# Kernel tuning notes

Hardware: AMD Instinct MI355X
Metric: run time of the kernel (lower is better)

The kernel has to match this reference:

```python
import jax, jax.numpy as jnp
import numpy as np

N = 100000      # nodes
E = 2000000     # edges
F_NODE = 32     # num_node_features
F_EDGE = 16     # num_edge_features
HID = 128       # size_conv_layers
G = 4096        # num graphs (molecules)
NCLS = 2        # class_weights.shape[0]
NEG = 0.01      # LeakyReLU default negative slope
BN_EPS = 1e-5


def _bn(h, gamma, beta):
    # torch BatchNorm1d training-mode forward: biased batch stats over node dim
    m = jnp.mean(h, axis=0)
    v = jnp.var(h, axis=0)
    return (h - m) * jax.lax.rsqrt(v + BN_EPS) * gamma + beta


def _lrelu(h):
    return jnp.where(h > 0, h, NEG * h)


def setup_inputs() -> dict:
    key = jax.random.key(0)
    ks = jax.random.split(key, 64)
    d = {}
    d["x"] = jax.random.normal(ks[0], (N, F_NODE), dtype=jnp.float32)
    d["edge_index"] = jax.random.randint(ks[1], (2, E), 0, N, dtype=jnp.int64)
    d["edge_attr"] = jax.random.normal(ks[2], (E, F_EDGE), dtype=jnp.float32)
    d["batch"] = jnp.sort(jax.random.randint(ks[3], (N,), 0, G, dtype=jnp.int64))
    dims = [F_NODE, HID, HID]  # in_channels of each conv layer
    i = 4
    for l, ic in enumerate(dims):
        d[f"eps{l}"] = jnp.zeros((), jnp.float32)                                # GINE train_eps init 0
        d[f"ew{l}"] = 0.05 * jax.random.normal(ks[i], (F_EDGE, ic), jnp.float32); i += 1
        d[f"eb{l}"] = jnp.zeros((ic,), jnp.float32)
        d[f"w1{l}"] = 0.05 * jax.random.normal(ks[i], (ic, HID), jnp.float32); i += 1
        d[f"b1{l}"] = jnp.zeros((HID,), jnp.float32)
        d[f"g1{l}"] = jnp.ones((HID,), jnp.float32)
        d[f"be1{l}"] = jnp.zeros((HID,), jnp.float32)
        d[f"w2{l}"] = 0.05 * jax.random.normal(ks[i], (HID, HID), jnp.float32); i += 1
        d[f"b2{l}"] = jnp.zeros((HID,), jnp.float32)
        d[f"g2{l}"] = jnp.ones((HID,), jnp.float32)
        d[f"be2{l}"] = jnp.zeros((HID,), jnp.float32)
    d["wf"] = 0.05 * jax.random.normal(ks[i], (2 * HID, NCLS), jnp.float32)
    d["bf"] = jnp.zeros((NCLS,), jnp.float32)
    return d


def _forward(x, edge_index, edge_attr, batch, layers, wf, bf):
    src = edge_index[0]  # x_j (messages flow source->target in PyG)
    dst = edge_index[1]  # x_i
    for (eps, ew, eb, w1, b1, g1, be1, w2, b2, g2, be2) in layers:
        e = edge_attr @ ew + eb                     # [E, in_ch]
        msg = jax.nn.relu(x[src] + e)               # GINE message
        agg = jax.ops.segment_sum(msg, dst, num_segments=N)
        h = (1.0 + eps) * x + agg                   # [N, in_ch]
        h = _lrelu(_bn(h @ w1 + b1, g1, be1))       # nn: Lin->BN->LeakyReLU
        h = h @ w2 + b2                             # nn: Lin
        x = _lrelu(_bn(h, g2, be2))                 # outer BN + LeakyReLU
    pool = jax.ops.segment_sum(x, batch, num_segments=G)  # global_add_pool
    x_cat = jnp.concatenate([x, pool[batch]], axis=1)      # repeat_interleave broadcast
    logits = x_cat @ wf + bf
    return jax.nn.softmax(logits, axis=1)


def reference(x, edge_index, edge_attr, batch,
              eps0, ew0, eb0, w10, b10, g10, be10, w20, b20, g20, be20,
              eps1, ew1, eb1, w11, b11, g11, be11, w21, b21, g21, be21,
              eps2, ew2, eb2, w12, b12, g12, be12, w22, b22, g22, be22,
              wf, bf):
    layers = [
        (eps0, ew0, eb0, w10, b10, g10, be10, w20, b20, g20, be20),
        (eps1, ew1, eb1, w11, b11, g11, be11, w21, b21, g21, be21),
        (eps2, ew2, eb2, w12, b12, g12, be12, w22, b22, g22, be22),
    ]
    return _forward(x, edge_index, edge_attr, batch, layers, wf, bf)
```

## Files before the change

### kernel.cpp

```cpp
#include <hip/hip_runtime.h>

#define GEMM_GRID 512
#define GNUM 4096

typedef __attribute__((ext_vector_type(8))) short short8_t;
typedef __attribute__((ext_vector_type(4))) float f32x4;
typedef __attribute__((ext_vector_type(2))) float v2f;

__device__ __forceinline__ float bf2f(unsigned short u) {
    union { unsigned int i; float f; } v; v.i = ((unsigned int)u) << 16; return v.f;
}
__device__ __forceinline__ unsigned short f2bf(float f) {
    union { float f; unsigned int i; } v; v.f = f;
    unsigned int b = v.i + 0x7FFFu + ((v.i >> 16) & 1u);
    return (unsigned short)(b >> 16);
}
__device__ __forceinline__ float lrelu(float v) { return v > 0.f ? v : 0.01f * v; }

__global__ __launch_bounds__(256) void hist_kernel(
    const int* __restrict__ dstv, int* __restrict__ cnt, int E)
{
    int i = blockIdx.x * 256 + threadIdx.x;
    if (i < E) atomicAdd(&cnt[dstv[i] + 1], 1);
}

__global__ __launch_bounds__(256) void scan_block_kernel(
    int* __restrict__ data, int* __restrict__ bsum, int n)
{
    __shared__ int s[256];
    int tid = threadIdx.x;
    int base = blockIdx.x * 1024 + tid * 4;
    int v[4]; int run = 0;
    #pragma unroll
    for (int i = 0; i < 4; i++) {
        int x = (base + i < n) ? data[base + i] : 0;
        run += x; v[i] = run;
    }
    s[tid] = run; __syncthreads();
    for (int off = 1; off < 256; off <<= 1) {
        int t = (tid >= off) ? s[tid - off] : 0;
        __syncthreads();
        s[tid] += t;
        __syncthreads();
    }
    int excl = s[tid] - run;
    #pragma unroll
    for (int i = 0; i < 4; i++)
        if (base + i < n) data[base + i] = v[i] + excl;
    if (tid == 255) bsum[blockIdx.x] = s[255];
}

__global__ __launch_bounds__(128) void scan_carry_kernel(int* __restrict__ bsum, int nb)
{
    __shared__ int s[128];
    int tid = threadIdx.x;
    int orig = (tid < nb) ? bsum[tid] : 0;
    s[tid] = orig; __syncthreads();
    for (int off = 1; off < 128; off <<= 1) {
        int t = (tid >= off) ? s[tid - off] : 0;
        __syncthreads();
        s[tid] += t;
        __syncthreads();
    }
    if (tid < nb) bsum[tid] = s[tid] - orig;
}

__global__ __launch_bounds__(256) void scan_add_kernel(
    int* __restrict__ data, const int* __restrict__ bsum,
    int* __restrict__ cursor, int n, int N)
{
    int i = blockIdx.x * 256 + threadIdx.x;
    if (i < n) {
        int v = data[i] + bsum[i >> 10];
        data[i] = v;
        if (i < N) cursor[i] = v;
    }
}

__global__ __launch_bounds__(256) void scatter_kernel(
    const int* __restrict__ dstv, int* __restrict__ cursor,
    int* __restrict__ perm, int E)
{
    int i = blockIdx.x * 256 + threadIdx.x;
    if (i < E) {
        int p = atomicAdd(&cursor[dstv[i]], 1);
        perm[p] = i;
    }
}

__global__ __launch_bounds__(256) void reorder_kernel(
    const float* __restrict__ ea, const int* __restrict__ srcv,
    const int* __restrict__ perm, float* __restrict__ eap,
    int* __restrict__ srcp, int E)
{
    int i = blockIdx.x * 256 + threadIdx.x;
    int p = i >> 2, q = i & 3;
    if (p >= E) return;
    int e = perm[p];
    float4 v = reinterpret_cast<const float4*>(ea)[e * 4 + q];
    reinterpret_cast<float4*>(eap)[p * 4 + q] = v;
    if (q == 0) srcp[p] = srcv[e];
}

template<bool RO>
__global__ __launch_bounds__(256) void gather_kernel32(
    const float* __restrict__ ea, const int* __restrict__ srcv,
    const int* __restrict__ perm, const int* __restrict__ off,
    const float* __restrict__ ew, const float* __restrict__ ebias,
    const float* __restrict__ epsp, const float* __restrict__ x,
    unsigned short* __restrict__ aggh, unsigned short* __restrict__ aggl, int N)
{
    __shared__ float ebuf[4][32 * 16];
    const int tid = threadIdx.x;
    const int wv = tid >> 6;
    const int lane = tid & 63;
    int n = __builtin_amdgcn_readfirstlane((int)((blockIdx.x * 256 + tid) >> 6));
    if (n >= N) return;
    const int h = lane >> 5;
    const int c = lane & 31;
    float ewr[16];
    #pragma unroll
    for (int k = 0; k < 16; k++) ewr[k] = ew[k * 32 + c];
    const float ebr = ebias[c];
    const float xself = x[(size_t)n * 32 + c];
    float acc = 0.f;
    const int p0 = off[n], end = off[n + 1];
    float* eb_ = ebuf[wv];
    const float4* eaq = reinterpret_cast<const float4*>(ea);

    for (int p = p0; p < end; p += 32) {
        int sv[16];
        #pragma unroll
        for (int j = 0; j < 16; j++) {
            int pj = min(p + h * 16 + j, end - 1);
            int e = RO ? pj : perm[pj];
            sv[j] = srcv[e];
        }
        int rowA = min(p + (lane >> 2), end - 1);
        int rowB = min(p + 16 + (lane >> 2), end - 1);
        int erA = RO ? rowA : perm[rowA];
        int erB = RO ? rowB : perm[rowB];
        float4 eaA = eaq[(size_t)erA * 4 + (lane & 3)];
        float4 eaB = eaq[(size_t)erB * 4 + (lane & 3)];
        __builtin_amdgcn_sched_barrier(0);
        float xv[16];
        #pragma unroll
        for (int j = 0; j < 16; j++)
            xv[j] = x[(size_t)sv[j] * 32 + c];
        __builtin_amdgcn_sched_barrier(0);
        __threadfence_block();
        *reinterpret_cast<float4*>(&eb_[(lane >> 2) * 16 + (lane & 3) * 4]) = eaA;
        *reinterpret_cast<float4*>(&eb_[(16 + (lane >> 2)) * 16 + (lane & 3) * 4]) = eaB;
        __threadfence_block();
        #pragma unroll
        for (int j = 0; j < 16; j++) {
            int row = h * 16 + j;
            const float4* er4 = reinterpret_cast<const float4*>(&eb_[row * 16]);
            float4 e0 = er4[0], e1 = er4[1], e2 = er4[2], e3 = er4[3];
            float u = ebr;
            u = fmaf(e0.x, ewr[0], u);  u = fmaf(e0.y, ewr[1], u);
            u = fmaf(e0.z, ewr[2], u);  u = fmaf(e0.w, ewr[3], u);
            u = fmaf(e1.x, ewr[4], u);  u = fmaf(e1.y, ewr[5], u);
            u = fmaf(e1.z, ewr[6], u);  u = fmaf(e1.w, ewr[7], u);
            u = fmaf(e2.x, ewr[8], u);  u = fmaf(e2.y, ewr[9], u);
            u = fmaf(e2.z, ewr[10], u); u = fmaf(e2.w, ewr[11], u);
            u = fmaf(e3.x, ewr[12], u); u = fmaf(e3.y, ewr[13], u);
            u = fmaf(e3.z, ewr[14], u); u = fmaf(e3.w, ewr[15], u);
            bool valid = (p + row) < end;
            acc += valid ? fmaxf(xv[j] + u, 0.f) : 0.f;
        }
    }
    acc += __shfl_xor(acc, 32);
    if (lane < 32) {
        float s = 1.f + epsp[0];
        float f = fmaf(xself, s, acc);
        unsigned int b = __float_as_uint(f);
        unsigned short hi = (unsigned short)(b >> 16);
        float lo = f - __uint_as_float(b & 0xffff0000u);
        aggh[(size_t)n * 32 + c] = hi;
        aggl[(size_t)n * 32 + c] = f2bf(lo);
    }
}

template<bool RO>
__global__ __launch_bounds__(256) void gather_kernel128_bn(
    const float* __restrict__ ea, const int* __restrict__ srcv,
    const int* __restrict__ perm, const int* __restrict__ off,
    const float* __restrict__ ew, const float* __restrict__ ebias,
    const float* __restrict__ epsp, const float* __restrict__ U,
    const float* __restrict__ stats, const float* __restrict__ g,
    const float* __restrict__ be, float invN,
    unsigned short* __restrict__ aggh, unsigned short* __restrict__ aggl, int N)
{
    int lane = threadIdx.x & 63;
    int n = __builtin_amdgcn_readfirstlane((int)((blockIdx.x * 256 + threadIdx.x) >> 6));
    if (n >= N) return;
    const int c0 = lane * 2;
    v2f scv, shv;
    {
        float m0 = stats[c0] * invN;
        float v0 = fmaxf(stats[128 + c0] * invN - m0 * m0, 0.f);
        scv.x = g[c0] * rsqrtf(v0 + 1e-5f);
        shv.x = be[c0] - m0 * scv.x;
        float m1 = stats[c0 + 1] * invN;
        float v1 = fmaxf(stats[128 + c0 + 1] * invN - m1 * m1, 0.f);
        scv.y = g[c0 + 1] * rsqrtf(v1 + 1e-5f);
        shv.y = be[c0 + 1] - m1 * scv.y;
    }
    v2f ewv[16];
    #pragma unroll
    for (int k = 0; k < 16; k++)
        ewv[k] = *reinterpret_cast<const v2f*>(&ew[k * 128 + c0]);
    const v2f ebv = *reinterpret_cast<const v2f*>(&ebias[c0]);
    const v2f xn = *reinterpret_cast<const v2f*>(&U[(size_t)n * 128 + c0]);
    v2f acc = {0.f, 0.f};
    const int p0 = off[n];
    const int end = off[n + 1];
    for (int p = p0; p < end; p += 4) {
        int ee[4]; bool vv[4];
        #pragma unroll
        for (int j = 0; j < 4; j++) {
            int pj = p + j;
            vv[j] = pj < end;
            int ij = vv[j] ? pj : p;
            ee[j] = RO ? ij : perm[ij];
        }
        int ss[4];
        #pragma unroll
        for (int j = 0; j < 4; j++) ss[j] = srcv[ee[j]];
        float4 at[4][4];
        #pragma unroll
        for (int j = 0; j < 4; j++) {
            const float4* ap = reinterpret_cast<const float4*>(ea + (size_t)ee[j] * 16);
            #pragma unroll
            for (int q = 0; q < 4; q++) at[j][q] = ap[q];
        }
        v2f xv[4];
        #pragma unroll
        for (int j = 0; j < 4; j++)
            xv[j] = *reinterpret_cast<const v2f*>(&U[(size_t)ss[j] * 128 + c0]);
        __builtin_amdgcn_sched_barrier(0);
        #pragma unroll
        for (int j = 0; j < 4; j++) {
            float av[16];
            #pragma unroll
            for (int q = 0; q < 4; q++) {
                av[4*q] = at[j][q].x; av[4*q+1] = at[j][q].y;
                av[4*q+2] = at[j][q].z; av[4*q+3] = at[j][q].w;
            }
            v2f xb = xv[j] * scv + shv;
            xb.x = lrelu(xb.x); xb.y = lrelu(xb.y);
            v2f u = ebv;
            #pragma unroll
            for (int k = 0; k < 16; k++) u = ewv[k] * av[k] + u;
            v2f m = xb + u;
            m.x = fmaxf(m.x, 0.f); m.y = fmaxf(m.y, 0.f);
            acc.x += vv[j] ? m.x : 0.f;
            acc.y += vv[j] ? m.y : 0.f;
        }
    }
    v2f xnb = xn * scv + shv;
    xnb.x = lrelu(xnb.x); xnb.y = lrelu(xnb.y);
    float s = 1.f + epsp[0];
    v2f o = xnb * s + acc;
    unsigned int b0 = __float_as_uint(o.x);
    unsigned int b1 = __float_as_uint(o.y);
    unsigned int hp = __builtin_amdgcn_perm(b1, b0, 0x07060302u);
    float l0 = o.x - __uint_as_float(b0 & 0xffff0000u);
    float l1 = o.y - __uint_as_float(b1 & 0xffff0000u);
    unsigned int lp = (unsigned int)f2bf(l0) | ((unsigned int)f2bf(l1) << 16);
    *reinterpret_cast<unsigned int*>(&aggh[(size_t)n * 128 + c0]) = hp;
    *reinterpret_cast<unsigned int*>(&aggl[(size_t)n * 128 + c0]) = lp;
}

template<int K>
__global__ __launch_bounds__(256, 3) void gemm_copy_mfma_kernel(
    const unsigned short* __restrict__ Ah, const unsigned short* __restrict__ Al,
    const float* __restrict__ W, const float* __restrict__ bias,
    float* __restrict__ out, float* __restrict__ stats_out, int N, int ntiles)
{
    constexpr int PA = K + 8;
    __shared__ unsigned short As_hi[32 * PA];
    __shared__ unsigned short As_lo[32 * PA];
    __shared__ unsigned short Wt[128 * PA];
    const int tid = threadIdx.x;
    const int w = tid >> 6;
    const int lane = tid & 63;
    const int quad = lane >> 4;
    const int l16 = lane & 15;
    const int rbase = (w & 1) * 16;
    const int nbase = (w >> 1) * 4;

    for (int idx = tid; idx < K * 128; idx += 256) {
        int k = idx >> 7, nn = idx & 127;
        Wt[nn * PA + k] = f2bf(W[idx]);
    }
    float bcol[4];
    #pragma unroll
    for (int nt = 0; nt < 4; nt++) bcol[nt] = bias[(nbase + nt) * 16 + l16];
    float csum[4] = {0.f, 0.f, 0.f, 0.f}, csq[4] = {0.f, 0.f, 0.f, 0.f};

    constexpr int C8 = K / 8;

    for (int tile = blockIdx.x; tile < ntiles; tile += gridDim.x) {
        const int row0 = tile * 32;
        __syncthreads();
        for (int cid = tid; cid < 32 * C8; cid += 256) {
            int row = cid / C8, c8 = cid % C8;
            int r = row0 + row;
            uint4 h, l;
            if (r < N) {
                h = *reinterpret_cast<const uint4*>(&Ah[(size_t)r * K + c8 * 8]);
                l = *reinterpret_cast<const uint4*>(&Al[(size_t)r * K + c8 * 8]);
            } else {
                h = make_uint4(0u,0u,0u,0u);
                l = make_uint4(0u,0u,0u,0u);
            }
            *reinterpret_cast<uint4*>(&As_hi[row * PA + c8 * 8]) = h;
            *reinterpret_cast<uint4*>(&As_lo[row * PA + c8 * 8]) = l;
        }
        __syncthreads();

        f32x4 acc[4];
        #pragma unroll
        for (int nt = 0; nt < 4; nt++) { f32x4 z = {0.f,0.f,0.f,0.f}; acc[nt] = z; }
        #pragma unroll
        for (int chunk = 0; chunk < K / 32; chunk++) {
            short8_t ahi = *reinterpret_cast<const short8_t*>(
                &As_hi[(rbase + l16) * PA + chunk * 32 + quad * 8]);
            short8_t alo = *reinterpret_cast<const short8_t*>(
                &As_lo[(rbase + l16) * PA + chunk * 32 + quad * 8]);
            #pragma unroll
            for (int nt = 0; nt < 4; nt++) {
                short8_t bfr = *reinterpret_cast<const short8_t*>(
                    &Wt[((nbase + nt) * 16 + l16) * PA + chunk * 32 + quad * 8]);
                acc[nt] = __builtin_amdgcn_mfma_f32_16x16x32_bf16(alo, bfr, acc[nt], 0, 0, 0);
                acc[nt] = __builtin_amdgcn_mfma_f32_16x16x32_bf16(ahi, bfr, acc[nt], 0, 0, 0);
            }
        }
        const int rb = row0 + rbase + quad * 4;
        #pragma unroll
        for (int nt = 0; nt < 4; nt++) {
            #pragma unroll
            for (int rg = 0; rg < 4; rg++) {
                int r = rb + rg;
                if (r < N) {
                    float v = acc[nt][rg] + bcol[nt];
                    out[(size_t)r * 128 + (nbase + nt) * 16 + l16] = v;
                    csum[nt] += v; csq[nt] += v * v;
                }
            }
        }
    }
    #pragma unroll
    for (int nt = 0; nt < 4; nt++) {
        float s = csum[nt]; s += __shfl_xor(s, 16); s += __shfl_xor(s, 32);
        float q = csq[nt];  q += __shfl_xor(q, 16); q += __shfl_xor(q, 32);
        if (quad == 0) {
            int col = (nbase + nt) * 16 + l16;
            atomicAdd(&stats_out[col], s);
            atomicAdd(&stats_out[128 + col], q);
        }
    }
}

__global__ __launch_bounds__(256, 3) void gemm_bn_mfma_kernel(
    const float* __restrict__ A,
    const float* __restrict__ stats_in, const float* __restrict__ g,
    const float* __restrict__ be, float invN,
    const float* __restrict__ W, const float* __restrict__ bias,
    float* __restrict__ out, float* __restrict__ stats_out, int N, int ntiles)
{
    constexpr int K = 128;
    constexpr int PA = K + 8;
    __shared__ unsigned short As_hi[32 * PA];
    __shared__ unsigned short As_lo[32 * PA];
    __shared__ unsigned short Wt[128 * PA];
    __shared__ float scale_s[K];
    __shared__ float shift_s[K];
    const int tid = threadIdx.x;
    const int w = tid >> 6;
    const int lane = tid & 63;
    const int quad = lane >> 4;
    const int l16 = lane & 15;
    const int rbase = (w & 1) * 16;
    const int nbase = (w >> 1) * 4;

    for (int idx = tid; idx < K * 128; idx += 256) {
        int k = idx >> 7, nn = idx & 127;
        Wt[nn * PA + k] = f2bf(W[idx]);
    }
    for (int i = tid; i < K; i += 256) {
        float m = stats_in[i] * invN;
        float va = fmaxf(stats_in[K + i] * invN - m * m, 0.f);
        float sc = g[i] * rsqrtf(va + 1e-5f);
        scale_s[i] = sc;
        shift_s[i] = be[i] - m * sc;
    }
    float bcol[4];
    #pragma unroll
    for (int nt = 0; nt < 4; nt++) bcol[nt] = bias[(nbase + nt) * 16 + l16];
    float csum[4] = {0.f, 0.f, 0.f, 0.f}, csq[4] = {0.f, 0.f, 0.f, 0.f};

    constexpr int C8 = K / 8;

    for (int tile = blockIdx.x; tile < ntiles; tile += gridDim.x) {
        const int row0 = tile * 32;
        __syncthreads();
        for (int cid = tid; cid < 32 * C8; cid += 256) {
            int row = cid / C8, c8 = cid % C8;
            int r = row0 + row;
            float f[8];
            if (r < N) {
                float4 u0 = *reinterpret_cast<const float4*>(&A[(size_t)r * K + c8 * 8]);
                float4 u1 = *reinterpret_cast<const float4*>(&A[(size_t)r * K + c8 * 8 + 4]);
                f[0]=u0.x; f[1]=u0.y; f[2]=u0.z; f[3]=u0.w;
                f[4]=u1.x; f[5]=u1.y; f[6]=u1.z; f[7]=u1.w;
            } else {
                #pragma unroll
                for (int j = 0; j < 8; j++) f[j] = 0.f;
            }
            int kb = c8 * 8;
            #pragma unroll
            for (int j = 0; j < 8; j++)
                f[j] = lrelu(fmaf(f[j], scale_s[kb + j], shift_s[kb + j]));
            unsigned int hi[4], lo[4];
            #pragma unroll
            for (int j = 0; j < 4; j++) {
                unsigned int b0 = __float_as_uint(f[2*j]);
                unsigned int b1 = __float_as_uint(f[2*j + 1]);
                hi[j] = __builtin_amdgcn_perm(b1, b0, 0x07060302u);
                float l0 = f[2*j]     - __uint_as_float(b0 & 0xffff0000u);
                float l1 = f[2*j + 1] - __uint_as_float(b1 & 0xffff0000u);
                lo[j] = __builtin_amdgcn_perm(__float_as_uint(l1), __float_as_uint(l0), 0x07060302u);
            }
            *reinterpret_cast<uint4*>(&As_hi[row * PA + c8 * 8]) = make_uint4(hi[0], hi[1], hi[2], hi[3]);
            *reinterpret_cast<uint4*>(&As_lo[row * PA + c8 * 8]) = make_uint4(lo[0], lo[1], lo[2], lo[3]);
        }
        __syncthreads();

        f32x4 acc[4];
        #pragma unroll
        for (int nt = 0; nt < 4; nt++) { f32x4 z = {0.f,0.f,0.f,0.f}; acc[nt] = z; }
        #pragma unroll
        for (int chunk = 0; chunk < K / 32; chunk++) {
            short8_t ahi = *reinterpret_cast<const short8_t*>(
                &As_hi[(rbase + l16) * PA + chunk * 32 + quad * 8]);
            short8_t alo = *reinterpret_cast<const short8_t*>(
                &As_lo[(rbase + l16) * PA + chunk * 32 + quad * 8]);
            #pragma unroll
            for (int nt = 0; nt < 4; nt++) {
                short8_t bfr = *reinterpret_cast<const short8_t*>(
                    &Wt[((nbase + nt) * 16 + l16) * PA + chunk * 32 + quad * 8]);
                acc[nt] = __builtin_amdgcn_mfma_f32_16x16x32_bf16(alo, bfr, acc[nt], 0, 0, 0);
                acc[nt] = __builtin_amdgcn_mfma_f32_16x16x32_bf16(ahi, bfr, acc[nt], 0, 0, 0);
            }
        }
        const int rb = row0 + rbase + quad * 4;
        #pragma unroll
        for (int nt = 0; nt < 4; nt++) {
            #pragma unroll
            for (int rg = 0; rg < 4; rg++) {
                int r = rb + rg;
                if (r < N) {
                    float v = acc[nt][rg] + bcol[nt];
                    out[(size_t)r * 128 + (nbase + nt) * 16 + l16] = v;
                    csum[nt] += v; csq[nt] += v * v;
                }
            }
        }
    }
    #pragma unroll
    for (int nt = 0; nt < 4; nt++) {
        float s = csum[nt]; s += __shfl_xor(s, 16); s += __shfl_xor(s, 32);
        float q = csq[nt];  q += __shfl_xor(q, 16); q += __shfl_xor(q, 32);
        if (quad == 0) {
            int col = (nbase + nt) * 16 + l16;
            atomicAdd(&stats_out[col], s);
            atomicAdd(&stats_out[128 + col], q);
        }
    }
}

__global__ __launch_bounds__(256) void pool_kernel_bn(
    const float* __restrict__ U, const int* __restrict__ batch,
    const float* __restrict__ stats, const float* __restrict__ g,
    const float* __restrict__ be, float invN,
    float* __restrict__ pool, int N)
{
    int w = (blockIdx.x * 256 + threadIdx.x) >> 6;
    int lane = threadIdx.x & 63;
    int n0 = w * 32;
    if (n0 >= N) return;
    int n1 = min(n0 + 32, N);
    int c0 = lane * 2;
    float sc0, sh0, sc1, sh1;
    {
        float m0 = stats[c0] * invN;
        float v0 = fmaxf(stats[128 + c0] * invN - m0 * m0, 0.f);
        sc0 = g[c0] * rsqrtf(v0 + 1e-5f);
        sh0 = be[c0] - m0 * sc0;
        float m1 = stats[c0 + 1] * invN;
        float v1 = fmaxf(stats[128 + c0 + 1] * invN - m1 * m1, 0.f);
        sc1 = g[c0 + 1] * rsqrtf(v1 + 1e-5f);
        sh1 = be[c0 + 1] - m1 * sc1;
    }
    float a0 = 0.f, a1 = 0.f;
    int cur = batch[n0];
    for (int n = n0; n < n1; ++n) {
        int b = batch[n];
        if (b != cur) {
            atomicAdd(&pool[(size_t)cur * 128 + c0], a0);
            atomicAdd(&pool[(size_t)cur * 128 + c0 + 1], a1);
            a0 = a1 = 0.f; cur = b;
        }
        float2 v = *reinterpret_cast<const float2*>(&U[(size_t)n * 128 + c0]);
        a0 += lrelu(fmaf(v.x, sc0, sh0));
        a1 += lrelu(fmaf(v.y, sc1, sh1));
    }
    atomicAdd(&pool[(size_t)cur * 128 + c0], a0);
    atomicAdd(&pool[(size_t)cur * 128 + c0 + 1], a1);
}

__global__ __launch_bounds__(256) void final_kernel_bn(
    const float* __restrict__ U, const float* __restrict__ pool,
    const int* __restrict__ batch,
    const float* __restrict__ stats, const float* __restrict__ g,
    const float* __restrict__ be, float invN,
    const float* __restrict__ wf, const float* __restrict__ bf,
    float* __restrict__ out, int N)
{
    __shared__ float wf_s[512];
    int tid = threadIdx.x;
    for (int i = tid; i < 512; i += 256) wf_s[i] = wf[i];
    __syncthreads();
    int wid = tid >> 6, lane = tid & 63;
    int n = blockIdx.x * 4 + wid;
    if (n >= N) return;
    int cA = lane, cB = 64 + lane;
    float scA, shA, scB, shB;
    {
        float mA = stats[cA] * invN;
        float vA = fmaxf(stats[128 + cA] * invN - mA * mA, 0.f);
        scA = g[cA] * rsqrtf(vA + 1e-5f);
        shA = be[cA] - mA * scA;
        float mB = stats[cB] * invN;
        float vB = fmaxf(stats[128 + cB] * invN - mB * mB, 0.f);
        scB = g[cB] * rsqrtf(vB + 1e-5f);
        shB = be[cB] - mB * scB;
    }
    int b = batch[n];
    float v0 = lrelu(fmaf(U[(size_t)n * 128 + cA], scA, shA));
    float v1 = lrelu(fmaf(U[(size_t)n * 128 + cB], scB, shB));
    float p0 = pool[(size_t)b * 128 + cA];
    float p1 = pool[(size_t)b * 128 + cB];
    float a0 = v0 * wf_s[lane * 2]       + v1 * wf_s[(64 + lane) * 2]
             + p0 * wf_s[(128 + lane) * 2] + p1 * wf_s[(192 + lane) * 2];
    float a1 = v0 * wf_s[lane * 2 + 1]       + v1 * wf_s[(64 + lane) * 2 + 1]
             + p0 * wf_s[(128 + lane) * 2 + 1] + p1 * wf_s[(192 + lane) * 2 + 1];
    #pragma unroll
    for (int off = 32; off >= 1; off >>= 1) {
        a0 += __shfl_down(a0, off);
        a1 += __shfl_down(a1, off);
    }
    if (lane == 0) {
        a0 += bf[0]; a1 += bf[1];
        float mx = fmaxf(a0, a1);
        float e0 = __expf(a0 - mx), e1 = __expf(a1 - mx);
        float inv = 1.f / (e0 + e1);
        out[(size_t)n * 2]     = e0 * inv;
        out[(size_t)n * 2 + 1] = e1 * inv;
    }
}

extern "C" void kernel_launch(void* const* d_in, const int* in_sizes, int n_in,
                              void* d_out, int out_size, void* d_ws, size_t ws_size,
                              hipStream_t stream)
{
    const float* x0    = (const float*)d_in[0];
    const int*   ei    = (const int*)d_in[1];
    const float* ea    = (const float*)d_in[2];
    const int*   batch = (const int*)d_in[3];
    const int E = in_sizes[1] / 2;
    const int N = in_sizes[3];
    const int* srcv = ei;
    const int* dstv = ei + E;
    const float* wf = (const float*)d_in[37];
    const float* bfp = (const float*)d_in[38];
    float* out = (float*)d_out;
    const float invN = 1.0f / (float)N;
    const int ntiles = (N + 31) / 32;

    const size_t base_f = (size_t)2 * N * 128 + (size_t)GNUM * 128 + 6 * 256
                        + (size_t)(N + 1) + (size_t)N + 128 + (size_t)E;
    const size_t full_f = base_f + (size_t)E * 16 + (size_t)E;
    const bool ro = (ws_size >= full_f * 4);

    float* ws = (float*)d_ws;
    size_t o = 0;
    float* xA    = ws + o; o += (size_t)N * 128;
    float* xB    = ws + o; o += (size_t)N * 128;
    float* eap   = ws + o; o += ro ? (size_t)E * 16 : 0;
    float* poolb = ws + o; o += (size_t)GNUM * 128;
    float* statsb= ws + o; o += 6 * 256;
    int* srcp    = (int*)(ws + o); o += ro ? (size_t)E : 0;
    int* off     = (int*)(ws + o); o += (size_t)(N + 1);
    int* cursor  = (int*)(ws + o); o += (size_t)N;
    int* bsumb   = (int*)(ws + o); o += 128;
    int* perm    = (int*)(ws + o);

    unsigned short* planeh = (unsigned short*)xB;

    hipMemsetAsync(off, 0, (size_t)(N + 1) * sizeof(int), stream);
    hipMemsetAsync(statsb, 0, (size_t)6 * 256 * sizeof(float), stream);
    hipMemsetAsync(poolb, 0, (size_t)GNUM * 128 * sizeof(float), stream);
    hist_kernel<<<(E + 255) / 256, 256, 0, stream>>>(dstv, off, E);
    const int n1 = N + 1;
    const int nb = (n1 + 1023) / 1024;
    scan_block_kernel<<<nb, 256, 0, stream>>>(off, bsumb, n1);
    scan_carry_kernel<<<1, 128, 0, stream>>>(bsumb, nb);
    scan_add_kernel<<<(n1 + 255) / 256, 256, 0, stream>>>(off, bsumb, cursor, n1, N);
    scatter_kernel<<<(E + 255) / 256, 256, 0, stream>>>(dstv, cursor, perm, E);
    if (ro)
        reorder_kernel<<<(E * 4 + 255) / 256, 256, 0, stream>>>(ea, srcv, perm, eap, srcp, E);

    const float* g_ea  = ro ? eap  : ea;
    const int*   g_src = ro ? srcp : srcv;
    const int gather_blocks = (N + 3) / 4;

    const float *pg = nullptr, *pbe = nullptr;
    float* pstats = nullptr;

    for (int l = 0; l < 3; l++) {
        const int C = (l == 0) ? 32 : 128;
        int bidx = 4 + l * 11;
        const float* epsp = (const float*)d_in[bidx + 0];
        const float* ew   = (const float*)d_in[bidx + 1];
        const float* eb   = (const float*)d_in[bidx + 2];
        const float* w1   = (const float*)d_in[bidx + 3];
        const float* b1   = (const float*)d_in[bidx + 4];
        const float* g1   = (const float*)d_in[bidx + 5];
        const float* be1  = (const float*)d_in[bidx + 6];
        const float* w2   = (const float*)d_in[bidx + 7];
        const float* b2   = (const float*)d_in[bidx + 8];
        const float* g2   = (const float*)d_in[bidx + 9];
        const float* be2  = (const float*)d_in[bidx + 10];
        float* st1 = statsb + (size_t)(l * 2) * 256;
        float* st2 = statsb + (size_t)(l * 2 + 1) * 256;

        unsigned short* ah = planeh;
        unsigned short* al = planeh + (size_t)N * C;

        if (l == 0) {
            if (ro) gather_kernel32<true><<<gather_blocks, 256, 0, stream>>>(
                        g_ea, g_src, perm, off, ew, eb, epsp, x0, ah, al, N);
            else    gather_kernel32<false><<<gather_blocks, 256, 0, stream>>>(
                        g_ea, g_src, perm, off, ew, eb, epsp, x0, ah, al, N);
            gemm_copy_mfma_kernel<32><<<GEMM_GRID, 256, 0, stream>>>(
                ah, al, w1, b1, xA, st1, N, ntiles);
        } else {
            if (ro) gather_kernel128_bn<true><<<gather_blocks, 256, 0, stream>>>(
                        g_ea, g_src, perm, off, ew, eb, epsp, xA,
                        pstats, pg, pbe, invN, ah, al, N);
            else    gather_kernel128_bn<false><<<gather_blocks, 256, 0, stream>>>(
                        g_ea, g_src, perm, off, ew, eb, epsp, xA,
                        pstats, pg, pbe, invN, ah, al, N);
            gemm_copy_mfma_kernel<128><<<GEMM_GRID, 256, 0, stream>>>(
                ah, al, w1, b1, xA, st1, N, ntiles);
        }
        gemm_bn_mfma_kernel<<<GEMM_GRID, 256, 0, stream>>>(
            xA, st1, g1, be1, invN, w2, b2, xA, st2, N, ntiles);
        pstats = st2; pg = g2; pbe = be2;
    }
    pool_kernel_bn<<<((N + 31) / 32 * 64 + 255) / 256, 256, 0, stream>>>(
        xA, batch, pstats, pg, pbe, invN, poolb, N);
    final_kernel_bn<<<(N + 3) / 4, 256, 0, stream>>>(
        xA, poolb, batch, pstats, pg, pbe, invN, wf, bfp, out, N);
}
```

Baseline: 1.362 ms.

## Stage edge attributes cooperatively in LDS and gather 32 edges per iteration

The 128-channel gather kernel now processes 32 edges per iteration instead of 4. Each wave loads the 32 edge-attribute rows cooperatively with one float4 per lane and stages them in a per-wave LDS buffer, instead of every lane redundantly loading all 16 floats of each edge. All 32 source-node feature loads are issued before any compute to raise memory-level parallelism. This costs higher register pressure (32 src indices plus 32 v2f values) and relies on wave-level ordering with block fences rather than barriers around the LDS buffer.

```diff
diff --git a/kernel.cpp b/kernel.cpp
--- a/kernel.cpp
+++ b/kernel.cpp
@@ -192,8 +192,11 @@
     const float* __restrict__ be, float invN,
     unsigned short* __restrict__ aggh, unsigned short* __restrict__ aggl, int N)
 {
-    int lane = threadIdx.x & 63;
-    int n = __builtin_amdgcn_readfirstlane((int)((blockIdx.x * 256 + threadIdx.x) >> 6));
+    __shared__ float ebuf[4][32 * 16];
+    const int tid = threadIdx.x;
+    const int wv = tid >> 6;
+    const int lane = tid & 63;
+    int n = __builtin_amdgcn_readfirstlane((int)((blockIdx.x * 256 + tid) >> 6));
     if (n >= N) return;
     const int c0 = lane * 2;
     v2f scv, shv;
@@ -216,47 +219,54 @@
     v2f acc = {0.f, 0.f};
     const int p0 = off[n];
     const int end = off[n + 1];
-    for (int p = p0; p < end; p += 4) {
-        int ee[4]; bool vv[4];
-        #pragma unroll
-        for (int j = 0; j < 4; j++) {
-            int pj = p + j;
-            vv[j] = pj < end;
-            int ij = vv[j] ? pj : p;
-            ee[j] = RO ? ij : perm[ij];
-        }
-        int ss[4];
-        #pragma unroll
-        for (int j = 0; j < 4; j++) ss[j] = srcv[ee[j]];
-        float4 at[4][4];
-        #pragma unroll
-        for (int j = 0; j < 4; j++) {
-            const float4* ap = reinterpret_cast<const float4*>(ea + (size_t)ee[j] * 16);
-            #pragma unroll
-            for (int q = 0; q < 4; q++) at[j][q] = ap[q];
-        }
-        v2f xv[4];
-        #pragma unroll
-        for (int j = 0; j < 4; j++)
-            xv[j] = *reinterpret_cast<const v2f*>(&U[(size_t)ss[j] * 128 + c0]);
+    const int endm1 = end - 1;
+    float* eb_ = ebuf[wv];
+    const float4* eaq = reinterpret_cast<const float4*>(ea);
+
+    for (int p = p0; p < end; p += 32) {
+        int sv[32];
+        #pragma unroll
+        for (int j = 0; j < 32; j++) {
+            int pj = min(p + j, endm1);
+            int e = RO ? pj : perm[pj];
+            sv[j] = srcv[e];
+        }
+        int rowA = min(p + (lane >> 2), endm1);
+        int rowB = min(p + 16 + (lane >> 2), endm1);
+        int erA = RO ? rowA : perm[rowA];
+        int erB = RO ? rowB : perm[rowB];
+        float4 eaA = eaq[(size_t)erA * 4 + (lane & 3)];
+        float4 eaB = eaq[(size_t)erB * 4 + (lane & 3)];
         __builtin_amdgcn_sched_barrier(0);
-        #pragma unroll
-        for (int j = 0; j < 4; j++) {
-            float av[16];
-            #pragma unroll
-            for (int q = 0; q < 4; q++) {
-                av[4*q] = at[j][q].x; av[4*q+1] = at[j][q].y;
-                av[4*q+2] = at[j][q].z; av[4*q+3] = at[j][q].w;
-            }
+        v2f xv[32];
+        #pragma unroll
+        for (int j = 0; j < 32; j++)
+            xv[j] = *reinterpret_cast<const v2f*>(&U[(size_t)sv[j] * 128 + c0]);
+        __builtin_amdgcn_sched_barrier(0);
+        __threadfence_block();
+        *reinterpret_cast<float4*>(&eb_[(lane >> 2) * 16 + (lane & 3) * 4]) = eaA;
+        *reinterpret_cast<float4*>(&eb_[(16 + (lane >> 2)) * 16 + (lane & 3) * 4]) = eaB;
+        __threadfence_block();
+        #pragma unroll
+        for (int j = 0; j < 32; j++) {
+            const float4* er4 = reinterpret_cast<const float4*>(&eb_[j * 16]);
+            float4 e0 = er4[0], e1 = er4[1], e2 = er4[2], e3 = er4[3];
+            v2f u = ebv;
+            u = ewv[0]  * e0.x + u;  u = ewv[1]  * e0.y + u;
+            u = ewv[2]  * e0.z + u;  u = ewv[3]  * e0.w + u;
+            u = ewv[4]  * e1.x + u;  u = ewv[5]  * e1.y + u;
+            u = ewv[6]  * e1.z + u;  u = ewv[7]  * e1.w + u;
+            u = ewv[8]  * e2.x + u;  u = ewv[9]  * e2.y + u;
+            u = ewv[10] * e2.z + u;  u = ewv[11] * e2.w + u;
+            u = ewv[12] * e3.x + u;  u = ewv[13] * e3.y + u;
+            u = ewv[14] * e3.z + u;  u = ewv[15] * e3.w + u;
             v2f xb = xv[j] * scv + shv;
             xb.x = lrelu(xb.x); xb.y = lrelu(xb.y);
-            v2f u = ebv;
-            #pragma unroll
-            for (int k = 0; k < 16; k++) u = ewv[k] * av[k] + u;
             v2f m = xb + u;
             m.x = fmaxf(m.x, 0.f); m.y = fmaxf(m.y, 0.f);
-            acc.x += vv[j] ? m.x : 0.f;
-            acc.y += vv[j] ? m.y : 0.f;
+            bool valid = (p + j) < end;
+            acc.x += valid ? m.x : 0.f;
+            acc.y += valid ? m.y : 0.f;
         }
     }
     v2f xnb = xn * scv + shv;
```

New measurement: 1.607 ms. +18.0%, slower.

## Compute per-edge edge-feature projection with split-bf16 MFMA in 128-wide gather kernel

Applied to the files above, without the earlier changes.

Restructures the 128-channel gather kernel so each wave handles 32 edges at a time and computes the edge_attr @ ew projection with 32x32x16 bf16 MFMA instructions. The FP32 precision is approximated with three hi/lo split products. It replaces 16 scalar FMAs per channel per edge with matrix instructions and changes the lane-to-channel mapping to 32 lanes by 4 channel tiles. In exchange it processes padded edges in blocks of 32, which wastes work on low-degree nodes (about 20 edges on average), and it uses more registers for the 32 source indices and the gathered values.

```diff
diff --git a/kernel.cpp b/kernel.cpp
--- a/kernel.cpp
+++ b/kernel.cpp
@@ -5,6 +5,7 @@
 
 typedef __attribute__((ext_vector_type(8))) short short8_t;
 typedef __attribute__((ext_vector_type(4))) float f32x4;
+typedef __attribute__((ext_vector_type(16))) float f32x16;
 typedef __attribute__((ext_vector_type(2))) float v2f;
 
 __device__ __forceinline__ float bf2f(unsigned short u) {
@@ -16,6 +17,23 @@
     return (unsigned short)(b >> 16);
 }
 __device__ __forceinline__ float lrelu(float v) { return v > 0.f ? v : 0.01f * v; }
+
+__device__ __forceinline__ void split8(const float4& a, const float4& b,
+                                       short8_t& hi, short8_t& lo)
+{
+    float f[8] = {a.x, a.y, a.z, a.w, b.x, b.y, b.z, b.w};
+    union { unsigned int u[4]; short8_t s; } H, L;
+    #pragma unroll
+    for (int i = 0; i < 4; i++) {
+        unsigned int b0 = __float_as_uint(f[2*i]);
+        unsigned int b1 = __float_as_uint(f[2*i+1]);
+        H.u[i] = __builtin_amdgcn_perm(b1, b0, 0x07060302u);
+        float l0 = f[2*i]   - __uint_as_float(b0 & 0xffff0000u);
+        float l1 = f[2*i+1] - __uint_as_float(b1 & 0xffff0000u);
+        L.u[i] = (unsigned int)f2bf(l0) | ((unsigned int)f2bf(l1) << 16);
+    }
+    hi = H.s; lo = L.s;
+}
 
 __global__ __launch_bounds__(256) void hist_kernel(
     const int* __restrict__ dstv, int* __restrict__ cnt, int E)
@@ -192,85 +210,110 @@
     const float* __restrict__ be, float invN,
     unsigned short* __restrict__ aggh, unsigned short* __restrict__ aggl, int N)
 {
-    int lane = threadIdx.x & 63;
-    int n = __builtin_amdgcn_readfirstlane((int)((blockIdx.x * 256 + threadIdx.x) >> 6));
+    const int tid = threadIdx.x;
+    const int lane = tid & 63;
+    int n = __builtin_amdgcn_readfirstlane((int)((blockIdx.x * 256 + tid) >> 6));
     if (n >= N) return;
-    const int c0 = lane * 2;
-    v2f scv, shv;
-    {
-        float m0 = stats[c0] * invN;
-        float v0 = fmaxf(stats[128 + c0] * invN - m0 * m0, 0.f);
-        scv.x = g[c0] * rsqrtf(v0 + 1e-5f);
-        shv.x = be[c0] - m0 * scv.x;
-        float m1 = stats[c0 + 1] * invN;
-        float v1 = fmaxf(stats[128 + c0 + 1] * invN - m1 * m1, 0.f);
-        scv.y = g[c0 + 1] * rsqrtf(v1 + 1e-5f);
-        shv.y = be[c0 + 1] - m1 * scv.y;
-    }
-    v2f ewv[16];
-    #pragma unroll
-    for (int k = 0; k < 16; k++)
-        ewv[k] = *reinterpret_cast<const v2f*>(&ew[k * 128 + c0]);
-    const v2f ebv = *reinterpret_cast<const v2f*>(&ebias[c0]);
-    const v2f xn = *reinterpret_cast<const v2f*>(&U[(size_t)n * 128 + c0]);
-    v2f acc = {0.f, 0.f};
-    const int p0 = off[n];
-    const int end = off[n + 1];
-    for (int p = p0; p < end; p += 4) {
-        int ee[4]; bool vv[4];
-        #pragma unroll
-        for (int j = 0; j < 4; j++) {
-            int pj = p + j;
-            vv[j] = pj < end;
-            int ij = vv[j] ? pj : p;
-            ee[j] = RO ? ij : perm[ij];
-        }
-        int ss[4];
-        #pragma unroll
-        for (int j = 0; j < 4; j++) ss[j] = srcv[ee[j]];
-        float4 at[4][4];
-        #pragma unroll
-        for (int j = 0; j < 4; j++) {
-            const float4* ap = reinterpret_cast<const float4*>(ea + (size_t)ee[j] * 16);
+    const int l31 = lane & 31;
+    const int h = lane >> 5;
+
+    float sc[4], sh[4], ebr[4], xnv[4];
+    #pragma unroll
+    for (int nt = 0; nt < 4; nt++) {
+        int c = nt * 32 + l31;
+        float m = stats[c] * invN;
+        float v = fmaxf(stats[128 + c] * invN - m * m, 0.f);
+        float s = g[c] * rsqrtf(v + 1e-5f);
+        sc[nt] = s; sh[nt] = be[c] - m * s;
+        ebr[nt] = ebias[c];
+        xnv[nt] = U[(size_t)n * 128 + c];
+    }
+    short8_t bwh[4], bwl[4];
+    #pragma unroll
+    for (int nt = 0; nt < 4; nt++) {
+        int c = nt * 32 + l31;
+        union { unsigned int u[4]; short8_t s; } H, L;
+        #pragma unroll
+        for (int i = 0; i < 4; i++) {
+            float f0 = ew[(h * 8 + 2 * i) * 128 + c];
+            float f1 = ew[(h * 8 + 2 * i + 1) * 128 + c];
+            unsigned int b0 = __float_as_uint(f0);
+            unsigned int b1 = __float_as_uint(f1);
+            H.u[i] = __builtin_amdgcn_perm(b1, b0, 0x07060302u);
+            float l0 = f0 - __uint_as_float(b0 & 0xffff0000u);
+            float l1 = f1 - __uint_as_float(b1 & 0xffff0000u);
+            L.u[i] = (unsigned int)f2bf(l0) | ((unsigned int)f2bf(l1) << 16);
+        }
+        bwh[nt] = H.s; bwl[nt] = L.s;
+    }
+
+    float accv[4] = {0.f, 0.f, 0.f, 0.f};
+    const int p0 = off[n], end = off[n + 1];
+    const int endm1 = end - 1;
+
+    for (int p = p0; p < end; p += 32) {
+        int sv[32];
+        #pragma unroll
+        for (int j = 0; j < 32; j++) {
+            int pj = min(p + j, endm1);
+            int e = RO ? pj : perm[pj];
+            sv[j] = srcv[e];
+        }
+        int rowp = min(p + l31, endm1);
+        int er = RO ? rowp : perm[rowp];
+        const float4* eap4 = reinterpret_cast<const float4*>(ea + (size_t)er * 16 + h * 8);
+        float4 fa = eap4[0], fb = eap4[1];
+        short8_t ah, al;
+        split8(fa, fb, ah, al);
+        __builtin_amdgcn_sched_barrier(0);
+        #pragma unroll
+        for (int np = 0; np < 2; np++) {
+            float xv0[16], xv1[16];
             #pragma unroll
-            for (int q = 0; q < 4; q++) at[j][q] = ap[q];
-        }
-        v2f xv[4];
-        #pragma unroll
-        for (int j = 0; j < 4; j++)
-            xv[j] = *reinterpret_cast<const v2f*>(&U[(size_t)ss[j] * 128 + c0]);
-        __builtin_amdgcn_sched_barrier(0);
-        #pragma unroll
-        for (int j = 0; j < 4; j++) {
-            float av[16];
+            for (int r = 0; r < 16; r++) {
+                int base = (r & 3) + (r >> 2) * 8;
+                int s = h ? sv[base + 4] : sv[base];
+                xv0[r] = U[(size_t)s * 128 + (np * 2) * 32 + l31];
+                xv1[r] = U[(size_t)s * 128 + (np * 2 + 1) * 32 + l31];
+            }
+            __builtin_amdgcn_sched_barrier(0);
             #pragma unroll
-            for (int q = 0; q < 4; q++) {
-                av[4*q] = at[j][q].x; av[4*q+1] = at[j][q].y;
-                av[4*q+2] = at[j][q].z; av[4*q+3] = at[j][q].w;
-            }
-            v2f xb = xv[j] * scv + shv;
-            xb.x = lrelu(xb.x); xb.y = lrelu(xb.y);
-            v2f u = ebv;
-            #pragma unroll
-            for (int k = 0; k < 16; k++) u = ewv[k] * av[k] + u;
-            v2f m = xb + u;
-            m.x = fmaxf(m.x, 0.f); m.y = fmaxf(m.y, 0.f);
-            acc.x += vv[j] ? m.x : 0.f;
-            acc.y += vv[j] ? m.y : 0.f;
-        }
-    }
-    v2f xnb = xn * scv + shv;
-    xnb.x = lrelu(xnb.x); xnb.y = lrelu(xnb.y);
-    float s = 1.f + epsp[0];
-    v2f o = xnb * s + acc;
-    unsigned int b0 = __float_as_uint(o.x);
-    unsigned int b1 = __float_as_uint(o.y);
-    unsigned int hp = __builtin_amdgcn_perm(b1, b0, 0x07060302u);
-    float l0 = o.x - __uint_as_float(b0 & 0xffff0000u);
-    float l1 = o.y - __uint_as_float(b1 & 0xffff0000u);
-    unsigned int lp = (unsigned int)f2bf(l0) | ((unsigned int)f2bf(l1) << 16);
-    *reinterpret_cast<unsigned int*>(&aggh[(size_t)n * 128 + c0]) = hp;
-    *reinterpret_cast<unsigned int*>(&aggl[(size_t)n * 128 + c0]) = lp;
+            for (int q = 0; q < 2; q++) {
+                int nt = np * 2 + q;
+                f32x16 c16;
+                #pragma unroll
+                for (int r = 0; r < 16; r++) c16[r] = ebr[nt];
+                c16 = __builtin_amdgcn_mfma_f32_32x32x16_bf16(ah, bwh[nt], c16, 0, 0, 0);
+                c16 = __builtin_amdgcn_mfma_f32_32x32x16_bf16(al, bwh[nt], c16, 0, 0, 0);
+                c16 = __builtin_amdgcn_mfma_f32_32x32x16_bf16(ah, bwl[nt], c16, 0, 0, 0);
+                float a = 0.f;
+                #pragma unroll
+                for (int r = 0; r < 16; r++) {
+                    int base = (r & 3) + (r >> 2) * 8;
+                    float xraw = q ? xv1[r] : xv0[r];
+                    float xb = lrelu(fmaf(xraw, sc[nt], sh[nt]));
+                    float m = fmaxf(xb + c16[r], 0.f);
+                    bool valid = (p + base + 4 * h) < end;
+                    a += valid ? m : 0.f;
+                }
+                accv[nt] += a;
+            }
+        }
+    }
+    #pragma unroll
+    for (int nt = 0; nt < 4; nt++) accv[nt] += __shfl_xor(accv[nt], 32);
+    const float s1e = 1.f + epsp[0];
+    if (lane < 32) {
+        #pragma unroll
+        for (int nt = 0; nt < 4; nt++) {
+            int c = nt * 32 + lane;
+            float xnb = lrelu(fmaf(xnv[nt], sc[nt], sh[nt]));
+            float o = fmaf(xnb, s1e, accv[nt]);
+            unsigned int b = __float_as_uint(o);
+            aggh[(size_t)n * 128 + c] = (unsigned short)(b >> 16);
+            aggl[(size_t)n * 128 + c] = f2bf(o - __uint_as_float(b & 0xffff0000u));
+        }
+    }
 }
 
 template<int K>
```

Result: slower. 1.833 ms (+34.5%).

## Fuse edge scatter with reorder and precompute bf16 transposed weights once

Applied to the files above, without the earlier changes.

Merges the counting-sort scatter and the edge-attribute/source reorder into one kernel that writes each edge directly to its sorted slot. This removes the perm write/read and a separate pass. Adds a one-time kernel that converts and transposes all six MLP weight matrices to bf16, so every GEMM block does vectorized copies instead of a per-block strided fp32-to-bf16 conversion. The weight buffer reuses the cursor workspace after scatter, and perm is no longer filled in the reorder path.

```diff
diff --git a/kernel.cpp b/kernel.cpp
--- a/kernel.cpp
+++ b/kernel.cpp
@@ -88,18 +88,42 @@
     }
 }
 
-__global__ __launch_bounds__(256) void reorder_kernel(
-    const float* __restrict__ ea, const int* __restrict__ srcv,
-    const int* __restrict__ perm, float* __restrict__ eap,
-    int* __restrict__ srcp, int E)
+__global__ __launch_bounds__(256) void scatter_reorder_kernel(
+    const int* __restrict__ dstv, const int* __restrict__ srcv,
+    const float* __restrict__ ea, int* __restrict__ cursor,
+    float* __restrict__ eap, int* __restrict__ srcp, int E)
 {
     int i = blockIdx.x * 256 + threadIdx.x;
-    int p = i >> 2, q = i & 3;
-    if (p >= E) return;
-    int e = perm[p];
-    float4 v = reinterpret_cast<const float4*>(ea)[e * 4 + q];
-    reinterpret_cast<float4*>(eap)[p * 4 + q] = v;
-    if (q == 0) srcp[p] = srcv[e];
+    if (i >= E) return;
+    int p = atomicAdd(&cursor[dstv[i]], 1);
+    srcp[p] = srcv[i];
+    const float4* s = reinterpret_cast<const float4*>(ea) + (size_t)i * 4;
+    float4* d = reinterpret_cast<float4*>(eap) + (size_t)p * 4;
+    float4 v0 = s[0], v1 = s[1], v2 = s[2], v3 = s[3];
+    d[0] = v0; d[1] = v1; d[2] = v2; d[3] = v3;
+}
+
+__global__ __launch_bounds__(256) void wconv_kernel(
+    const float* __restrict__ w10, const float* __restrict__ w20,
+    const float* __restrict__ w11, const float* __restrict__ w21,
+    const float* __restrict__ w12, const float* __restrict__ w22,
+    unsigned short* __restrict__ wt)
+{
+    int idx = blockIdx.x * 256 + threadIdx.x;
+    if (idx < 4096) {
+        int nn = idx >> 5, k = idx & 31;
+        wt[idx] = f2bf(w10[k * 128 + nn]);
+        return;
+    }
+    int r = idx - 4096;
+    int seg = r >> 14;
+    if (seg >= 5) return;
+    int o = r & 16383;
+    int nn = o >> 7, k = o & 127;
+    const float* w = (seg == 0) ? w20 : (seg == 1) ? w11 : (seg == 2) ? w21
+                   : (seg == 3) ? w12 : w22;
+    wt[4096 + seg * 16384 + o] = f2bf(w[k * 128 + nn]);
+    (void)nn;
 }
 
 template<bool RO>
@@ -276,7 +300,7 @@
 template<int K>
 __global__ __launch_bounds__(256, 3) void gemm_copy_mfma_kernel(
     const unsigned short* __restrict__ Ah, const unsigned short* __restrict__ Al,
-    const float* __restrict__ W, const float* __restrict__ bias,
+    const unsigned short* __restrict__ Wpre, const float* __restrict__ bias,
     float* __restrict__ out, float* __restrict__ stats_out, int N, int ntiles)
 {
     constexpr int PA = K + 8;
@@ -291,16 +315,16 @@
     const int rbase = (w & 1) * 16;
     const int nbase = (w >> 1) * 4;
 
-    for (int idx = tid; idx < K * 128; idx += 256) {
-        int k = idx >> 7, nn = idx & 127;
-        Wt[nn * PA + k] = f2bf(W[idx]);
+    constexpr int C8 = K / 8;
+    for (int idx = tid; idx < 128 * C8; idx += 256) {
+        int nn = idx / C8, c8 = idx % C8;
+        *reinterpret_cast<uint4*>(&Wt[nn * PA + c8 * 8]) =
+            *reinterpret_cast<const uint4*>(&Wpre[nn * K + c8 * 8]);
     }
     float bcol[4];
     #pragma unroll
     for (int nt = 0; nt < 4; nt++) bcol[nt] = bias[(nbase + nt) * 16 + l16];
     float csum[4] = {0.f, 0.f, 0.f, 0.f}, csq[4] = {0.f, 0.f, 0.f, 0.f};
-
-    constexpr int C8 = K / 8;
 
     for (int tile = blockIdx.x; tile < ntiles; tile += gridDim.x) {
         const int row0 = tile * 32;
@@ -368,7 +392,7 @@
     const float* __restrict__ A,
     const float* __restrict__ stats_in, const float* __restrict__ g,
     const float* __restrict__ be, float invN,
-    const float* __restrict__ W, const float* __restrict__ bias,
+    const unsigned short* __restrict__ Wpre, const float* __restrict__ bias,
     float* __restrict__ out, float* __restrict__ stats_out, int N, int ntiles)
 {
     constexpr int K = 128;
@@ -386,9 +410,11 @@
     const int rbase = (w & 1) * 16;
     const int nbase = (w >> 1) * 4;
 
-    for (int idx = tid; idx < K * 128; idx += 256) {
-        int k = idx >> 7, nn = idx & 127;
-        Wt[nn * PA + k] = f2bf(W[idx]);
+    constexpr int C8 = K / 8;
+    for (int idx = tid; idx < 128 * C8; idx += 256) {
+        int nn = idx / C8, c8 = idx % C8;
+        *reinterpret_cast<uint4*>(&Wt[nn * PA + c8 * 8]) =
+            *reinterpret_cast<const uint4*>(&Wpre[nn * K + c8 * 8]);
     }
     for (int i = tid; i < K; i += 256) {
         float m = stats_in[i] * invN;
@@ -401,8 +427,6 @@
     #pragma unroll
     for (int nt = 0; nt < 4; nt++) bcol[nt] = bias[(nbase + nt) * 16 + l16];
     float csum[4] = {0.f, 0.f, 0.f, 0.f}, csq[4] = {0.f, 0.f, 0.f, 0.f};
-
-    constexpr int C8 = K / 8;
 
     for (int tile = blockIdx.x; tile < ntiles; tile += gridDim.x) {
         const int row0 = tile * 32;
@@ -610,6 +634,7 @@
     int* perm    = (int*)(ws + o);
 
     unsigned short* planeh = (unsigned short*)xB;
+    unsigned short* wtbuf = (unsigned short*)cursor;
 
     hipMemsetAsync(off, 0, (size_t)(N + 1) * sizeof(int), stream);
     hipMemsetAsync(statsb, 0, (size_t)6 * 256 * sizeof(float), stream);
@@ -620,9 +645,20 @@
     scan_block_kernel<<<nb, 256, 0, stream>>>(off, bsumb, n1);
     scan_carry_kernel<<<1, 128, 0, stream>>>(bsumb, nb);
     scan_add_kernel<<<(n1 + 255) / 256, 256, 0, stream>>>(off, bsumb, cursor, n1, N);
-    scatter_kernel<<<(E + 255) / 256, 256, 0, stream>>>(dstv, cursor, perm, E);
     if (ro)
-        reorder_kernel<<<(E * 4 + 255) / 256, 256, 0, stream>>>(ea, srcv, perm, eap, srcp, E);
+        scatter_reorder_kernel<<<(E + 255) / 256, 256, 0, stream>>>(
+            dstv, srcv, ea, cursor, eap, srcp, E);
+    else
+        scatter_kernel<<<(E + 255) / 256, 256, 0, stream>>>(dstv, cursor, perm, E);
+
+    wconv_kernel<<<(86016 + 255) / 256, 256, 0, stream>>>(
+        (const float*)d_in[4 + 3], (const float*)d_in[4 + 7],
+        (const float*)d_in[15 + 3], (const float*)d_in[15 + 7],
+        (const float*)d_in[26 + 3], (const float*)d_in[26 + 7], wtbuf);
+    const unsigned short* w1p[3] = { wtbuf, wtbuf + 4096 + 16384,
+                                     wtbuf + 4096 + 3 * 16384 };
+    const unsigned short* w2p[3] = { wtbuf + 4096, wtbuf + 4096 + 2 * 16384,
+                                     wtbuf + 4096 + 4 * 16384 };
 
     const float* g_ea  = ro ? eap  : ea;
     const int*   g_src = ro ? srcp : srcv;
@@ -637,11 +673,9 @@
         const float* epsp = (const float*)d_in[bidx + 0];
         const float* ew   = (const float*)d_in[bidx + 1];
         const float* eb   = (const float*)d_in[bidx + 2];
-        const float* w1   = (const float*)d_in[bidx + 3];
         const float* b1   = (const float*)d_in[bidx + 4];
         const float* g1   = (const float*)d_in[bidx + 5];
         const float* be1  = (const float*)d_in[bidx + 6];
-        const float* w2   = (const float*)d_in[bidx + 7];
         const float* b2   = (const float*)d_in[bidx + 8];
         const float* g2   = (const float*)d_in[bidx + 9];
         const float* be2  = (const float*)d_in[bidx + 10];
@@ -657,7 +691,7 @@
             else    gather_kernel32<false><<<gather_blocks, 256, 0, stream>>>(
                         g_ea, g_src, perm, off, ew, eb, epsp, x0, ah, al, N);
             gemm_copy_mfma_kernel<32><<<GEMM_GRID, 256, 0, stream>>>(
-                ah, al, w1, b1, xA, st1, N, ntiles);
+                ah, al, w1p[0], b1, xA, st1, N, ntiles);
         } else {
             if (ro) gather_kernel128_bn<true><<<gather_blocks, 256, 0, stream>>>(
                         g_ea, g_src, perm, off, ew, eb, epsp, xA,
@@ -666,10 +700,10 @@
                         g_ea, g_src, perm, off, ew, eb, epsp, xA,
                         pstats, pg, pbe, invN, ah, al, N);
             gemm_copy_mfma_kernel<128><<<GEMM_GRID, 256, 0, stream>>>(
-                ah, al, w1, b1, xA, st1, N, ntiles);
+                ah, al, w1p[l], b1, xA, st1, N, ntiles);
         }
         gemm_bn_mfma_kernel<<<GEMM_GRID, 256, 0, stream>>>(
-            xA, st1, g1, be1, invN, w2, b2, xA, st2, N, ntiles);
+            xA, st1, g1, be1, invN, w2p[l], b2, xA, st2, N, ntiles);
         pstats = st2; pg = g2; pbe = be2;
     }
     pool_kernel_bn<<<((N + 31) / 32 * 64 + 255) / 256, 256, 0, stream>>>(
```

Measured after the change: 1.234 ms (median of 2 runs). -9.4%, faster.
